# Kernel tuning notes

Hardware: AMD Instinct MI355X
Metric: run time of the kernel (lower is better)

The kernel has to match this reference:

```python
import jax, jax.numpy as jnp
import numpy as np

KSIZE = 7
NSPIX = 196


def _unfold(x, k):
    # x: (T, C, H, W) -> (T, C, k*k, H, W), reflect padding, torch Unfold ordering
    p = (k - 1) // 2
    T, C, H, W = x.shape
    xp = jnp.pad(x, ((0, 0), (0, 0), (p, p), (p, p)), mode='reflect')
    return jnp.stack([xp[:, :, i:i + H, j:j + W] for i in range(k) for j in range(k)], axis=2)


def setup_inputs() -> dict:
    key = jax.random.key(0)
    k1, k2, k3, k4, k5 = jax.random.split(key, 5)
    T, C, H, W = 2, 64, 160, 160
    fan_in = C * KSIZE * KSIZE
    x = jax.random.normal(k1, (T, C, H, W), jnp.float32)
    spix = jax.random.randint(k2, (T, H, W), 0, NSPIX, jnp.int32)
    W_lin = jax.random.normal(k3, (C, fan_in), jnp.float32) / np.sqrt(fan_in)
    b_lin = jax.random.normal(k4, (C,), jnp.float32) * 0.01
    w_scale = jax.random.normal(k5, (C,), jnp.float32) / np.sqrt(C)
    b_scale = jnp.zeros((1,), jnp.float32)
    return {"x": x, "spix": spix, "W_lin": W_lin, "b_lin": b_lin,
            "w_scale": w_scale, "b_scale": b_scale}


def reference(x, spix, W_lin, b_lin, w_scale, b_scale):
    T, C, H, W = x.shape
    K2 = KSIZE * KSIZE
    O = W_lin.shape[0]
    p = (KSIZE - 1) // 2

    # unfold(x) with reflect padding -> patches (T, C, K2, H, W)
    patches = _unfold(x, KSIZE)

    # unfold(spix) -> neighbor superpixel ids per pixel (T, K2, H, W)
    sp = jnp.pad(spix, ((0, 0), (p, p), (p, p)), mode='reflect')
    nb = jnp.stack([sp[:, i:i + H, j:j + W] for i in range(KSIZE) for j in range(KSIZE)], axis=1)

    # per-frame superpixel mean pooling (bist.get_pooled_video): down (T, S, C)
    seg = (spix.astype(jnp.int32) + jnp.arange(T, dtype=jnp.int32)[:, None, None] * NSPIX).reshape(-1)
    feats = x.transpose(0, 2, 3, 1).reshape(-1, C)  # (T*H*W, C)
    sums = jax.ops.segment_sum(feats, seg, num_segments=T * NSPIX).reshape(T, NSPIX, C)
    cnts = jax.ops.segment_sum(jnp.ones((seg.shape[0],), x.dtype), seg,
                               num_segments=T * NSPIX).reshape(T, NSPIX, 1)
    down = sums / jnp.maximum(cnts, 1.0)

    # squared pairwise distances between superpixel means: pwd (T, S, S)
    sq = jnp.sum(down * down, axis=-1)
    pwd = jnp.maximum(sq[:, :, None] + sq[:, None, :]
                      - 2.0 * jnp.einsum('tsc,tuc->tsu', down, down), 0.0)

    # sims[t,k,h,w] = ||mean(spix[t,h,w]) - mean(nb[t,k,h,w])||^2
    tidx = jnp.arange(T)[:, None, None, None]
    sims = pwd[tidx, spix[:, None, :, :], nb]  # (T, K2, H, W)

    # scale = 10 * softplus(1x1-conv(x / ||x||_c))  -> (T, H, W)
    xn = x / (jnp.linalg.norm(x, axis=1, keepdims=True) + 1e-10)
    scale = 10.0 * jax.nn.softplus(jnp.einsum('c,tchw->thw', w_scale, xn) + b_scale[0])

    # apply_norm 'exp_max' over the kernel-tap axis
    rw = jnp.exp(-scale[:, None, :, :] * sims)  # (T, K2, H, W)
    rw = rw / (1e-5 + jnp.max(rw, axis=1, keepdims=True))

    # dynamic conv: out[t,o,h,w] = sum_{c,k} W[o,c,k] * patches[t,c,k,h,w] * rw[t,k,h,w] + b[o]
    out = jnp.einsum('ock,tckhw,tkhw->tohw', W_lin.reshape(O, C, K2), patches, rw)
    return out + b_lin[None, :, None, None]
```

## Files before the change

### kernel.cpp

```cpp
#include <hip/hip_runtime.h>
#include <math.h>

#define TT 2
#define CC 64
#define HH 160
#define WW 160
#define KS 7
#define K2 49
#define NSPIX 196
#define HWSZ (HH*WW)
#define PAD 3
#define OO 64
#define FANIN (CC*K2)
#define TS 8
#define PS (TS+KS-1)
#define NPOS (PS*PS)

#define NCHUNK 50
#define CHUNKPIX 512

typedef _Float16 half8 __attribute__((ext_vector_type(8)));
typedef float f32x16 __attribute__((ext_vector_type(16)));
typedef unsigned int uint4v __attribute__((ext_vector_type(4)));
typedef _Float16 half2v __attribute__((ext_vector_type(2)));

__device__ __forceinline__ int reflect(int i, int n) {
    if (i < 0) i = -i;
    if (i >= n) i = 2*n - 2 - i;
    return i;
}

__global__ __launch_bounds__(256) void k_prep(const float* __restrict__ x,
                                              const int* __restrict__ spix,
                                              const float* __restrict__ Wl,
                                              const float* __restrict__ wsc,
                                              const float* __restrict__ bsc,
                                              float* __restrict__ sums,
                                              float* __restrict__ cnts,
                                              float* __restrict__ scale,
                                              _Float16* __restrict__ Wb,
                                              _Float16* __restrict__ xT) {
    __shared__ float ls[8*200];
    __shared__ float lcnt[200];
    int bid = blockIdx.x;
    int tid = threadIdx.x;

    if (bid < 800) {
        int cg = bid & 7;
        int rest = bid >> 3;
        int ch = rest % NCHUNK;
        int t  = rest / NCHUNK;

        for (int i = tid; i < 8*200; i += 256) ls[i] = 0.f;
        if (cg == 0) for (int i = tid; i < 200; i += 256) lcnt[i] = 0.f;
        __syncthreads();

        int base = ch*CHUNKPIX;
        const float* xb = x + ((size_t)t*CC + cg*8)*HWSZ;
        #pragma unroll
        for (int i = 0; i < CHUNKPIX; i += 256) {
            int pix = base + i + tid;
            int s = spix[t*HWSZ + pix];
            if (cg == 0) atomicAdd(&lcnt[s], 1.0f);
            #pragma unroll
            for (int j = 0; j < 8; ++j) atomicAdd(&ls[j*200 + s], xb[(size_t)j*HWSZ + pix]);
        }
        __syncthreads();

        float* sb = sums + (size_t)t*NSPIX*CC + cg*8;
        for (int i = tid; i < 8*NSPIX; i += 256) {
            int s = i >> 3, j = i & 7;
            float v = ls[j*200 + s];
            if (v != 0.f) atomicAdd(&sb[s*CC + j], v);
        }
        if (cg == 0)
            for (int i = tid; i < NSPIX; i += 256) {
                float v = lcnt[i];
                if (v != 0.f) atomicAdd(&cnts[t*NSPIX + i], v);
            }
    } else if (bid < 1000) {
        int pix = (bid - 800)*256 + tid;
        int t = pix / HWSZ, hw = pix - t*HWSZ;
        const float* xs = x + (size_t)t*CC*HWSZ + hw;
        float s1 = 0.f, s2 = 0.f;
        unsigned int pk[32];
        #pragma unroll
        for (int cp = 0; cp < 32; ++cp) {
            float v0 = xs[(size_t)(2*cp)*HWSZ];
            float v1 = xs[(size_t)(2*cp + 1)*HWSZ];
            s1 += wsc[2*cp]*v0 + wsc[2*cp+1]*v1;
            s2 = fmaf(v0, v0, s2); s2 = fmaf(v1, v1, s2);
            half2v h; h[0] = (_Float16)v0; h[1] = (_Float16)v1;
            pk[cp] = __builtin_bit_cast(unsigned int, h);
        }
        float z = s1/(sqrtf(s2) + 1e-10f) + bsc[0];
        float sp_ = (z > 0.f) ? z + log1pf(expf(-z)) : log1pf(expf(z));
        scale[pix] = 10.f*sp_;
        uint4v* dst = (uint4v*)(xT + (size_t)pix*64);
        #pragma unroll
        for (int q = 0; q < 8; ++q) {
            uint4v v = { pk[4*q], pk[4*q+1], pk[4*q+2], pk[4*q+3] };
            dst[q] = v;
        }
    } else {
        int row = (bid - 1000)*256 + tid;
        if (row < 2*K2*4*64) {
            int ln  = row & 63;
            int kc  = (row >> 6) & 3;
            int tq  = row >> 8;
            int tap = tq % K2;
            int qo  = tq / K2;
            int o = qo*32 + (ln & 31);
            int cb = kc*16 + (ln >> 5)*8;
            _Float16* dst = Wb + (size_t)row*8;
            const float* src = Wl + (size_t)o*FANIN + tap;
            #pragma unroll
            for (int j = 0; j < 8; ++j) dst[j] = (_Float16)src[(size_t)(cb + j)*K2];
        }
    }
}

__global__ __launch_bounds__(256) void k_pwd(const float* __restrict__ sums,
                                             const float* __restrict__ cnts,
                                             float* __restrict__ pwd) {
    int tid = blockIdx.x*256 + threadIdx.x;
    if (tid >= TT*NSPIX*NSPIX) return;
    int t = tid / (NSPIX*NSPIX); int r = tid - t*NSPIX*NSPIX;
    int s = r / NSPIX, u = r - (r / NSPIX)*NSPIX;
    const float* ds = sums + (size_t)(t*NSPIX + s)*CC;
    const float* du = sums + (size_t)(t*NSPIX + u)*CC;
    float is = 1.0f / fmaxf(cnts[t*NSPIX + s], 1.0f);
    float iu = 1.0f / fmaxf(cnts[t*NSPIX + u], 1.0f);
    float acc = 0.f;
    #pragma unroll 8
    for (int c = 0; c < CC; ++c) {
        float d = ds[c]*is - du[c]*iu;
        acc = fmaf(d, d, acc);
    }
    pwd[tid] = acc;
}

__global__ __launch_bounds__(256, 4) void k_main(
    const _Float16* __restrict__ xT, const int* __restrict__ spix,
    const _Float16* __restrict__ Wb, const float* __restrict__ b_lin,
    const float* __restrict__ pwd, const float* __restrict__ scale,
    float* __restrict__ out)
{
    __shared__ unsigned short xpT[NPOS*64];
    __shared__ unsigned short rwb[K2*64];
    __shared__ int   sp[NPOS];
    __shared__ float mxp[4*64];
    __shared__ float mxl[64];

    int bid = blockIdx.x;
    int t = bid / 400;
    int r = bid - t*400;
    int th0 = (r / 20)*TS, tw0 = (r - (r/20)*20)*TS;
    int tid = threadIdx.y*64 + threadIdx.x;

    for (int i = tid; i < NPOS; i += 256) {
        int rr = reflect(th0 + i/PS - PAD, HH);
        int cc = reflect(tw0 + i%PS - PAD, WW);
        sp[i] = spix[t*HWSZ + rr*WW + cc];
    }
    {
        const _Float16* xt = xT + (size_t)t*HWSZ*64;
        for (int i = tid; i < NPOS*8; i += 256) {
            int pos = i >> 3, cb = i & 7;
            int rr = reflect(th0 + pos/PS - PAD, HH);
            int cc = reflect(tw0 + pos%PS - PAD, WW);
            uint4v v = *(const uint4v*)(xt + (size_t)(rr*WW + cc)*64 + cb*8);
            int chunk = cb ^ (pos & 7);
            *(uint4v*)&xpT[pos*64 + chunk*8] = v;
        }
    }
    __syncthreads();

    int p_ = threadIdx.x;
    int ty = threadIdx.y;
    int py0 = p_ >> 3, px0 = p_ & 7;
    {
        float sc = scale[t*HWSZ + (th0 + py0)*WW + (tw0 + px0)];
        int s0 = sp[(py0 + PAD)*PS + (px0 + PAD)];
        const float* pr = pwd + (t*NSPIX + s0)*NSPIX;
        float pmax = 0.f;
        for (int k = ty; k < K2; k += 4) {
            int di = k/KS, dj = k - di*KS;
            int nb = sp[(py0 + di)*PS + (px0 + dj)];
            float v = expf(-sc * pr[nb]);
            rwb[k*64 + p_] = __builtin_bit_cast(unsigned short, (_Float16)v);
            pmax = fmaxf(pmax, v);
        }
        mxp[ty*64 + p_] = pmax;
    }
    __syncthreads();
    if (ty == 0) {
        float m = fmaxf(fmaxf(mxp[p_], mxp[64 + p_]), fmaxf(mxp[128 + p_], mxp[192 + p_]));
        mxl[p_] = 1.f/(1e-5f + m);
    }
    __syncthreads();
    {
        float s = mxl[p_];
        for (int k = ty; k < K2; k += 4) {
            float v = (float)__builtin_bit_cast(_Float16, rwb[k*64 + p_]) * s;
            rwb[k*64 + p_] = __builtin_bit_cast(unsigned short, (_Float16)v);
        }
    }
    __syncthreads();

    int ln = threadIdx.x;
    int wv = __builtin_amdgcn_readfirstlane(threadIdx.y);
    int qp = wv & 1, kh = wv >> 1;
    int p  = qp*32 + (ln & 31);
    int ppy = p >> 3, ppx = p & 7;
    int lhi = ln >> 5;

    int jc0 = 4*kh + lhi, jc1 = jc0 + 2;

    const _Float16* A0b = Wb + (size_t)(2*kh)*512 + ln*8;
    const _Float16* A1b = A0b + (size_t)K2*4*512;

    f32x16 acc0, acc1;
    #pragma unroll
    for (int i = 0; i < 16; ++i) { acc0[i] = 0.f; acc1[i] = 0.f; }

    int di = 0, dj = 0;
    #pragma unroll 7
    for (int tap = 0; tap < K2; ++tap) {
        const _Float16* a0 = A0b + (size_t)tap*2048;
        half8 A00 = *(const half8*)(a0);
        half8 A01 = *(const half8*)(a0 + 512);
        const _Float16* a1 = A1b + (size_t)tap*2048;
        half8 A10 = *(const half8*)(a1);
        half8 A11 = *(const half8*)(a1 + 512);

        int pos = (ppy + di)*PS + (ppx + dj);
        int sw  = pos & 7;
        const unsigned short* bbase = &xpT[pos*64];
        half8 B0 = *(const half8*)(bbase + ((jc0 ^ sw) << 3));
        half8 B1 = *(const half8*)(bbase + ((jc1 ^ sw) << 3));

        _Float16 rv = __builtin_bit_cast(_Float16, rwb[tap*64 + p]);
        half8 rv8 = { rv, rv, rv, rv, rv, rv, rv, rv };
        B0 *= rv8;
        B1 *= rv8;

        acc0 = __builtin_amdgcn_mfma_f32_32x32x16_f16(A00, B0, acc0, 0, 0, 0);
        acc0 = __builtin_amdgcn_mfma_f32_32x32x16_f16(A01, B1, acc0, 0, 0, 0);
        acc1 = __builtin_amdgcn_mfma_f32_32x32x16_f16(A10, B0, acc1, 0, 0, 0);
        acc1 = __builtin_amdgcn_mfma_f32_32x32x16_f16(A11, B1, acc1, 0, 0, 0);

        if (++dj == KS) { dj = 0; ++di; }
    }

    __syncthreads();
    float* red = (float*)xpT;
    if (kh == 1) {
        #pragma unroll
        for (int i = 0; i < 16; ++i) {
            red[((qp*2 + 0)*16 + i)*64 + ln] = acc0[i];
            red[((qp*2 + 1)*16 + i)*64 + ln] = acc1[i];
        }
    }
    __syncthreads();
    if (kh == 0) {
        int h = th0 + ppy, w = tw0 + ppx;
        int row_hi = 4*lhi;
        float* ob = out + (size_t)t*OO*HWSZ + h*WW + w;
        #pragma unroll
        for (int rg = 0; rg < 16; ++rg) {
            int o0 = (rg & 3) + 8*(rg >> 2) + row_hi;
            int o1 = 32 + o0;
            float v0 = acc0[rg] + red[((qp*2 + 0)*16 + rg)*64 + ln];
            float v1 = acc1[rg] + red[((qp*2 + 1)*16 + rg)*64 + ln];
            ob[(size_t)o0*HWSZ] = v0 + b_lin[o0];
            ob[(size_t)o1*HWSZ] = v1 + b_lin[o1];
        }
    }
}

extern "C" void kernel_launch(void* const* d_in, const int* in_sizes, int n_in,
                              void* d_out, int out_size, void* d_ws, size_t ws_size,
                              hipStream_t stream) {
    const float* x    = (const float*)d_in[0];
    const int*   spix = (const int*)d_in[1];
    const float* Wl   = (const float*)d_in[2];
    const float* bl   = (const float*)d_in[3];
    const float* wsc  = (const float*)d_in[4];
    const float* bsc  = (const float*)d_in[5];
    float* out = (float*)d_out;

    float* ws    = (float*)d_ws;
    float* sums  = ws;
    float* cnts  = sums + TT*NSPIX*CC;
    float* pwd   = cnts + TT*NSPIX;
    float* scale = pwd  + TT*NSPIX*NSPIX;
    _Float16* Wb = (_Float16*)(scale + TT*HWSZ);
    _Float16* xT = Wb + (size_t)2*K2*4*64*8;

    hipMemsetAsync(sums, 0, (size_t)(TT*NSPIX*CC + TT*NSPIX)*sizeof(float), stream);

    k_prep<<<1196, 256, 0, stream>>>(x, spix, Wl, wsc, bsc, sums, cnts, scale, Wb, xT);
    k_pwd <<<(TT*NSPIX*NSPIX + 255)/256, 256, 0, stream>>>(sums, cnts, pwd);

    dim3 blk(64, 4, 1);
    k_main<<<TT*400, blk, 0, stream>>>(xT, spix, Wb, bl, pwd, scale, out);
}
```

Baseline: 151.8 us.

## Defer max-normalization to epilogue, software-pipeline MFMA tap loop, enlarge pooling chunks

The per-pixel exp_max normalization moves out of the shared-memory rewrite pass and becomes a single multiply on the accumulated output, which removes two barriers and a full rwb pass. The tap loop is software-pipelined: the next tap's weight and patch operands are prefetched while the current MFMAs run, and the reweight scalar is stored as a packed half2. The pooling stage uses 1024-pixel chunks with half as many blocks, and expf becomes __expf. Risks are higher register pressure under the 4-waves launch bound, unnormalized fp16 weights before scaling, and more atomic serialization per pooling block.

```diff
diff --git a/kernel.cpp b/kernel.cpp
--- a/kernel.cpp
+++ b/kernel.cpp
@@ -16,8 +16,8 @@
 #define PS (TS+KS-1)
 #define NPOS (PS*PS)
 
-#define NCHUNK 50
-#define CHUNKPIX 512
+#define NCHUNK 25
+#define CHUNKPIX 1024
 
 typedef _Float16 half8 __attribute__((ext_vector_type(8)));
 typedef float f32x16 __attribute__((ext_vector_type(16)));
@@ -45,7 +45,7 @@
     int bid = blockIdx.x;
     int tid = threadIdx.x;
 
-    if (bid < 800) {
+    if (bid < 400) {
         int cg = bid & 7;
         int rest = bid >> 3;
         int ch = rest % NCHUNK;
@@ -78,8 +78,8 @@
                 float v = lcnt[i];
                 if (v != 0.f) atomicAdd(&cnts[t*NSPIX + i], v);
             }
-    } else if (bid < 1000) {
-        int pix = (bid - 800)*256 + tid;
+    } else if (bid < 600) {
+        int pix = (bid - 400)*256 + tid;
         int t = pix / HWSZ, hw = pix - t*HWSZ;
         const float* xs = x + (size_t)t*CC*HWSZ + hw;
         float s1 = 0.f, s2 = 0.f;
@@ -103,7 +103,7 @@
             dst[q] = v;
         }
     } else {
-        int row = (bid - 1000)*256 + tid;
+        int row = (bid - 600)*256 + tid;
         if (row < 2*K2*4*64) {
             int ln  = row & 63;
             int kc  = (row >> 6) & 3;
@@ -147,10 +147,9 @@
     float* __restrict__ out)
 {
     __shared__ unsigned short xpT[NPOS*64];
-    __shared__ unsigned short rwb[K2*64];
+    __shared__ unsigned int   rwb[K2*64];
     __shared__ int   sp[NPOS];
     __shared__ float mxp[4*64];
-    __shared__ float mxl[64];
 
     int bid = blockIdx.x;
     int t = bid / 400;
@@ -187,24 +186,13 @@
         for (int k = ty; k < K2; k += 4) {
             int di = k/KS, dj = k - di*KS;
             int nb = sp[(py0 + di)*PS + (px0 + dj)];
-            float v = expf(-sc * pr[nb]);
-            rwb[k*64 + p_] = __builtin_bit_cast(unsigned short, (_Float16)v);
+            float v = __expf(-sc * pr[nb]);
+            _Float16 h = (_Float16)v;
+            half2v hp; hp[0] = h; hp[1] = h;
+            rwb[k*64 + p_] = __builtin_bit_cast(unsigned int, hp);
             pmax = fmaxf(pmax, v);
         }
         mxp[ty*64 + p_] = pmax;
-    }
-    __syncthreads();
-    if (ty == 0) {
-        float m = fmaxf(fmaxf(mxp[p_], mxp[64 + p_]), fmaxf(mxp[128 + p_], mxp[192 + p_]));
-        mxl[p_] = 1.f/(1e-5f + m);
-    }
-    __syncthreads();
-    {
-        float s = mxl[p_];
-        for (int k = ty; k < K2; k += 4) {
-            float v = (float)__builtin_bit_cast(_Float16, rwb[k*64 + p_]) * s;
-            rwb[k*64 + p_] = __builtin_bit_cast(unsigned short, (_Float16)v);
-        }
     }
     __syncthreads();
 
@@ -217,40 +205,61 @@
 
     int jc0 = 4*kh + lhi, jc1 = jc0 + 2;
 
-    const _Float16* A0b = Wb + (size_t)(2*kh)*512 + ln*8;
-    const _Float16* A1b = A0b + (size_t)K2*4*512;
+    const _Float16* a0p = Wb + (size_t)(2*kh)*512 + ln*8;
+    const _Float16* a1p = a0p + (size_t)K2*4*512;
 
     f32x16 acc0, acc1;
     #pragma unroll
     for (int i = 0; i < 16; ++i) { acc0[i] = 0.f; acc1[i] = 0.f; }
 
+    half8 A00 = *(const half8*)(a0p);
+    half8 A01 = *(const half8*)(a0p + 512);
+    half8 A10 = *(const half8*)(a1p);
+    half8 A11 = *(const half8*)(a1p + 512);
+    int pos0 = ppy*PS + ppx;
+    int sw0  = pos0 & 7;
+    const unsigned short* bb0 = &xpT[pos0*64];
+    half8 B0 = *(const half8*)(bb0 + ((jc0 ^ sw0) << 3));
+    half8 B1 = *(const half8*)(bb0 + ((jc1 ^ sw0) << 3));
+    unsigned int rv = rwb[p];
+
     int di = 0, dj = 0;
-    #pragma unroll 7
-    for (int tap = 0; tap < K2; ++tap) {
-        const _Float16* a0 = A0b + (size_t)tap*2048;
-        half8 A00 = *(const half8*)(a0);
-        half8 A01 = *(const half8*)(a0 + 512);
-        const _Float16* a1 = A1b + (size_t)tap*2048;
-        half8 A10 = *(const half8*)(a1);
-        half8 A11 = *(const half8*)(a1 + 512);
-
-        int pos = (ppy + di)*PS + (ppx + dj);
-        int sw  = pos & 7;
-        const unsigned short* bbase = &xpT[pos*64];
-        half8 B0 = *(const half8*)(bbase + ((jc0 ^ sw) << 3));
-        half8 B1 = *(const half8*)(bbase + ((jc1 ^ sw) << 3));
-
-        _Float16 rv = __builtin_bit_cast(_Float16, rwb[tap*64 + p]);
-        half8 rv8 = { rv, rv, rv, rv, rv, rv, rv, rv };
-        B0 *= rv8;
-        B1 *= rv8;
-
-        acc0 = __builtin_amdgcn_mfma_f32_32x32x16_f16(A00, B0, acc0, 0, 0, 0);
-        acc0 = __builtin_amdgcn_mfma_f32_32x32x16_f16(A01, B1, acc0, 0, 0, 0);
-        acc1 = __builtin_amdgcn_mfma_f32_32x32x16_f16(A10, B0, acc1, 0, 0, 0);
-        acc1 = __builtin_amdgcn_mfma_f32_32x32x16_f16(A11, B1, acc1, 0, 0, 0);
-
+    #pragma unroll 8
+    for (int tap = 0; tap < K2 - 1; ++tap) {
         if (++dj == KS) { dj = 0; ++di; }
+        a0p += 2048; a1p += 2048;
+        half8 nA00 = *(const half8*)(a0p);
+        half8 nA01 = *(const half8*)(a0p + 512);
+        half8 nA10 = *(const half8*)(a1p);
+        half8 nA11 = *(const half8*)(a1p + 512);
+        int npos = (ppy + di)*PS + (ppx + dj);
+        int nsw  = npos & 7;
+        const unsigned short* nbb = &xpT[npos*64];
+        half8 nB0 = *(const half8*)(nbb + ((jc0 ^ nsw) << 3));
+        half8 nB1 = *(const half8*)(nbb + ((jc1 ^ nsw) << 3));
+        unsigned int nrv = rwb[(tap + 1)*64 + p];
+
+        half2v rh = __builtin_bit_cast(half2v, rv);
+        half8 rv8 = { rh[0], rh[1], rh[0], rh[1], rh[0], rh[1], rh[0], rh[1] };
+        half8 b0 = B0 * rv8;
+        half8 b1 = B1 * rv8;
+        acc0 = __builtin_amdgcn_mfma_f32_32x32x16_f16(A00, b0, acc0, 0, 0, 0);
+        acc1 = __builtin_amdgcn_mfma_f32_32x32x16_f16(A10, b0, acc1, 0, 0, 0);
+        acc0 = __builtin_amdgcn_mfma_f32_32x32x16_f16(A01, b1, acc0, 0, 0, 0);
+        acc1 = __builtin_amdgcn_mfma_f32_32x32x16_f16(A11, b1, acc1, 0, 0, 0);
+
+        A00 = nA00; A01 = nA01; A10 = nA10; A11 = nA11;
+        B0 = nB0; B1 = nB1; rv = nrv;
+    }
+    {
+        half2v rh = __builtin_bit_cast(half2v, rv);
+        half8 rv8 = { rh[0], rh[1], rh[0], rh[1], rh[0], rh[1], rh[0], rh[1] };
+        half8 b0 = B0 * rv8;
+        half8 b1 = B1 * rv8;
+        acc0 = __builtin_amdgcn_mfma_f32_32x32x16_f16(A00, b0, acc0, 0, 0, 0);
+        acc1 = __builtin_amdgcn_mfma_f32_32x32x16_f16(A10, b0, acc1, 0, 0, 0);
+        acc0 = __builtin_amdgcn_mfma_f32_32x32x16_f16(A01, b1, acc0, 0, 0, 0);
+        acc1 = __builtin_amdgcn_mfma_f32_32x32x16_f16(A11, b1, acc1, 0, 0, 0);
     }
 
     __syncthreads();
@@ -264,6 +273,8 @@
     }
     __syncthreads();
     if (kh == 0) {
+        float m = fmaxf(fmaxf(mxp[p], mxp[64 + p]), fmaxf(mxp[128 + p], mxp[192 + p]));
+        float s = 1.f/(1e-5f + m);
         int h = th0 + ppy, w = tw0 + ppx;
         int row_hi = 4*lhi;
         float* ob = out + (size_t)t*OO*HWSZ + h*WW + w;
@@ -273,8 +284,8 @@
             int o1 = 32 + o0;
             float v0 = acc0[rg] + red[((qp*2 + 0)*16 + rg)*64 + ln];
             float v1 = acc1[rg] + red[((qp*2 + 1)*16 + rg)*64 + ln];
-            ob[(size_t)o0*HWSZ] = v0 + b_lin[o0];
-            ob[(size_t)o1*HWSZ] = v1 + b_lin[o1];
+            ob[(size_t)o0*HWSZ] = v0*s + b_lin[o0];
+            ob[(size_t)o1*HWSZ] = v1*s + b_lin[o1];
         }
     }
 }
@@ -300,7 +311,7 @@
 
     hipMemsetAsync(sums, 0, (size_t)(TT*NSPIX*CC + TT*NSPIX)*sizeof(float), stream);
 
-    k_prep<<<1196, 256, 0, stream>>>(x, spix, Wl, wsc, bsc, sums, cnts, scale, Wb, xT);
+    k_prep<<<698, 256, 0, stream>>>(x, spix, Wl, wsc, bsc, sums, cnts, scale, Wb, xT);
     k_pwd <<<(TT*NSPIX*NSPIX + 255)/256, 256, 0, stream>>>(sums, cnts, pwd);
 
     dim3 blk(64, 4, 1);
```

Result: no change. 150.4 us (-0.9%).
